# Performance work log

Hardware: AMD Instinct MI355X
Metric: run time of the kernel (lower is better)

The kernel has to match this reference:

```python
import jax, jax.numpy as jnp
import numpy as np

B, N, IN, H, OUT = 128, 8192, 9, 128, 9


def setup_inputs() -> dict:
    key = jax.random.key(0)
    ks = jax.random.split(key, 4)
    y = jax.random.normal(ks[0], (B, N, 6), dtype=jnp.float32)
    W1 = jax.random.normal(ks[1], (IN, H), dtype=jnp.float32) / np.sqrt(IN)
    b1 = jnp.zeros((H,), dtype=jnp.float32)
    W2 = jax.random.normal(ks[2], (H, H), dtype=jnp.float32) / np.sqrt(H)
    b2 = jnp.zeros((H,), dtype=jnp.float32)
    W3 = jax.random.normal(ks[3], (H, OUT), dtype=jnp.float32) / np.sqrt(H)
    b3 = jnp.zeros((OUT,), dtype=jnp.float32)
    return {"y": y, "W1": W1, "b1": b1, "W2": W2, "b2": b2, "W3": W3, "b3": b3}


def _make_triplets(coords):
    # coords: (B, N, 3) -> (B, N-2, 9) = (a1, a2, a3, x1, y1, x2, y2, x3, y3)
    xp = coords[:, :-2, :]
    xm = coords[:, 1:-1, :]
    xn = coords[:, 2:, :]
    off = jnp.arctan2(xm[..., 1] - xp[..., 1], xm[..., 0] - xp[..., 0])
    return jnp.stack(
        (xp[..., 2] - off, xm[..., 2] - off, xn[..., 2] - off,
         xp[..., 0], xp[..., 1], xm[..., 0], xm[..., 1], xn[..., 0], xn[..., 1]),
        axis=-1,
    )


def reference(y, W1, b1, W2, b2, W3, b3):
    coords = y[..., :3]                      # (B, N, 3)
    t = _make_triplets(coords)               # (B, N-2, 9)
    h = jax.nn.swish(t @ W1 + b1)            # (B, N-2, H)
    h = jax.nn.swish(h @ W2 + b2)            # (B, N-2, H)
    f = h @ W3 + b3                          # (B, N-2, 9)
    # overlap-add scatter back onto the N cycles
    res = jnp.zeros_like(coords)
    res = res.at[:, :-2, :].add(jnp.stack([f[..., 3], f[..., 4], f[..., 0]], axis=-1))
    res = res.at[:, 1:-1, :].add(jnp.stack([f[..., 5], f[..., 6], f[..., 1]], axis=-1))
    res = res.at[:, 2:, :].add(jnp.stack([f[..., 7], f[..., 8], f[..., 2]], axis=-1))
    # boundaries = (1, 1): clamp both ends
    res = res.at[:, 0, :].set(0.0)
    res = res.at[:, -1, :].set(0.0)
    return res
```

## Files before the change

kernel.cpp:

```cpp
#include <hip/hip_runtime.h>
#include <hip/hip_bf16.h>

#define Bn 128
#define Nn 8192
#define Hn 128
#define RPB 128
#define JOUT 126
#define NBJ 66

typedef __attribute__((ext_vector_type(8))) short short8;
typedef __attribute__((ext_vector_type(4))) float f32x4;
typedef __attribute__((ext_vector_type(4))) unsigned int u32x4;

__device__ __forceinline__ unsigned short f2bf(float x) {
    union { float f; unsigned u; } v; v.f = x;
    return (unsigned short)((v.u + 0x7fffu + ((v.u >> 16) & 1u)) >> 16);
}
__device__ __forceinline__ float bf2f(unsigned short h) {
    union { unsigned u; float f; } v; v.u = ((unsigned)h) << 16;
    return v.f;
}
__device__ __forceinline__ unsigned short flo(float x) {
    return f2bf(x - bf2f(f2bf(x)));
}
__device__ __forceinline__ float swish(float x) {
    return x * __builtin_amdgcn_rcpf(1.0f + __expf(-x));
}
__device__ __forceinline__ unsigned pk2(float a, float b) {
    union { __hip_bfloat16 h; unsigned short u; } ca, cb;
    ca.h = __float2bfloat16(a); cb.h = __float2bfloat16(b);
    return (unsigned)ca.u | ((unsigned)cb.u << 16);
}

__global__ void prep_kernel(const float* __restrict__ W1, const float* __restrict__ b1,
                            const float* __restrict__ W2, const float* __restrict__ W3,
                            unsigned short* __restrict__ ws)
{
    int tid = blockIdx.x * 256 + threadIdx.x;
    if (tid >= 22528) return;
    int f = tid >> 9, r = tid & 511;
    int l = r >> 3, e = r & 7;
    int p = ((l >> 4) << 3) | e;
    int c16 = l & 15;
    unsigned short v = 0;
    if (f < 8) {
        int col = (f << 4) | c16;
        if (p < 9)        v = f2bf(W1[p * Hn + col]);
        else if (p < 18)  v = flo(W1[(p - 9) * Hn + col]);
        else if (p < 27)  v = f2bf(W1[(p - 18) * Hn + col]);
        else if (p == 27) v = f2bf(b1[col]);
        else if (p == 28) v = flo(b1[col]);
    } else if (f < 40) {
        int mt2 = (f - 8) >> 2, ks = (f - 8) & 3;
        int col = (mt2 << 4) | c16;
        int k = 16 * (2 * ks + ((p & 7) >> 2)) + ((p >> 3) << 2) + (p & 3);
        v = f2bf(W2[k * Hn + col]);
    } else {
        int ks = f - 40;
        int k = 16 * (2 * ks + ((p & 7) >> 2)) + ((p >> 3) << 2) + (p & 3);
        if (c16 < 9) v = f2bf(W3[k * 9 + c16]);
    }
    ws[tid] = v;
}

__global__ __launch_bounds__(256, 4) void fused_kernel(
    const float* __restrict__ y, const float* __restrict__ b2g,
    const float* __restrict__ b3, const unsigned short* __restrict__ ws,
    float* __restrict__ out)
{
    __shared__ __align__(16) char tb[RPB * 80];
    __shared__ float f_lds[RPB][12];

    const int tid = threadIdx.x;
    const int lane = tid & 63;
    const int w = tid >> 6;
    const int b = blockIdx.y;
    const int j0 = blockIdx.x * JOUT;
    const int r15 = lane & 15, g = lane >> 4;

    const short8* wsf = (const short8*)ws;

    if (tid < RPB) {
        int i = j0 - 2 + tid;
        i = (i < 0) ? 0 : ((i > Nn - 3) ? (Nn - 3) : i);
        const float* base = y + ((size_t)b * Nn + i) * 6;
        float xp0 = base[0],  xp1 = base[1],  xp2 = base[2];
        float xm0 = base[6],  xm1 = base[7],  xm2 = base[8];
        float xn0 = base[12], xn1 = base[13], xn2 = base[14];
        float off = atan2f(xm1 - xp1, xm0 - xp0);
        float t0 = xp2 - off, t1 = xm2 - off, t2 = xn2 - off;
        unsigned short h0 = f2bf(t0), h1 = f2bf(t1), h2 = f2bf(t2);
        unsigned short h3 = f2bf(xp0), h4 = f2bf(xp1), h5 = f2bf(xm0);
        unsigned short h6 = f2bf(xm1), h7 = f2bf(xn0), h8 = f2bf(xn1);
        unsigned short l0 = f2bf(t0 - bf2f(h0)), l1 = f2bf(t1 - bf2f(h1));
        unsigned short l2 = f2bf(t2 - bf2f(h2)), l3 = f2bf(xp0 - bf2f(h3));
        unsigned short l4 = f2bf(xp1 - bf2f(h4)), l5 = f2bf(xm0 - bf2f(h5));
        unsigned short l6 = f2bf(xm1 - bf2f(h6)), l7 = f2bf(xn0 - bf2f(h7));
        unsigned short l8 = f2bf(xn1 - bf2f(h8));
        #define PK(a,bv) ((unsigned)(a) | ((unsigned)(bv) << 16))
        u32x4 v0 = { PK(h0,h1), PK(h2,h3), PK(h4,h5), PK(h6,h7) };
        u32x4 v1 = { PK(h8,h0), PK(h1,h2), PK(h3,h4), PK(h5,h6) };
        u32x4 v2 = { PK(h7,h8), PK(l0,l1), PK(l2,l3), PK(l4,l5) };
        u32x4 v3 = { PK(l6,l7), PK(l8,0x3F80u), PK(0x3F80u,0u), 0u };
        #undef PK
        char* dst = tb + tid * 80;
        *(u32x4*)(dst)      = v0;
        *(u32x4*)(dst + 16) = v1;
        *(u32x4*)(dst + 32) = v2;
        *(u32x4*)(dst + 48) = v3;
    }
    __syncthreads();

    short8 b2f[2][4];
    {
        short8 w1f[8];
        #pragma unroll
        for (int mt = 0; mt < 8; ++mt) w1f[mt] = wsf[mt * 64 + lane];
        #pragma unroll
        for (int nt = 0; nt < 2; ++nt) {
            short8 tf = *(const short8*)(tb + (32 * w + 16 * nt + r15) * 80 + g * 16);
            f32x4 acc1[8];
            #pragma unroll
            for (int mt = 0; mt < 8; ++mt)
                acc1[mt] = __builtin_amdgcn_mfma_f32_16x16x32_bf16(w1f[mt], tf, (f32x4)0.0f, 0, 0, 0);
            #pragma unroll
            for (int ks = 0; ks < 4; ++ks) {
                union { unsigned u[4]; short8 s; } pk;
                pk.u[0] = pk2(swish(acc1[2 * ks][0]),     swish(acc1[2 * ks][1]));
                pk.u[1] = pk2(swish(acc1[2 * ks][2]),     swish(acc1[2 * ks][3]));
                pk.u[2] = pk2(swish(acc1[2 * ks + 1][0]), swish(acc1[2 * ks + 1][1]));
                pk.u[3] = pk2(swish(acc1[2 * ks + 1][2]), swish(acc1[2 * ks + 1][3]));
                b2f[nt][ks] = pk.s;
            }
        }
    }

    unsigned a3u[2][4][4];
    #pragma unroll
    for (int mt2 = 0; mt2 < 8; ++mt2) {
        short8 a2f0 = wsf[512 + (mt2 * 4 + 0) * 64 + lane];
        short8 a2f1 = wsf[512 + (mt2 * 4 + 1) * 64 + lane];
        short8 a2f2 = wsf[512 + (mt2 * 4 + 2) * 64 + lane];
        short8 a2f3 = wsf[512 + (mt2 * 4 + 3) * 64 + lane];
        const f32x4 bias = *(const f32x4*)(b2g + mt2 * 16 + 4 * g);
        #pragma unroll
        for (int nt = 0; nt < 2; ++nt) {
            f32x4 acc = __builtin_amdgcn_mfma_f32_16x16x32_bf16(a2f0, b2f[nt][0], (f32x4)0.0f, 0, 0, 0);
            acc = __builtin_amdgcn_mfma_f32_16x16x32_bf16(a2f1, b2f[nt][1], acc, 0, 0, 0);
            acc = __builtin_amdgcn_mfma_f32_16x16x32_bf16(a2f2, b2f[nt][2], acc, 0, 0, 0);
            acc = __builtin_amdgcn_mfma_f32_16x16x32_bf16(a2f3, b2f[nt][3], acc, 0, 0, 0);
            float s0 = swish(acc[0] + bias[0]);
            float s1 = swish(acc[1] + bias[1]);
            float s2 = swish(acc[2] + bias[2]);
            float s3 = swish(acc[3] + bias[3]);
            a3u[nt][mt2 >> 1][(mt2 & 1) * 2 + 0] = pk2(s0, s1);
            a3u[nt][mt2 >> 1][(mt2 & 1) * 2 + 1] = pk2(s2, s3);
        }
    }

    {
        short8 b3f[4];
        #pragma unroll
        for (int ks = 0; ks < 4; ++ks) b3f[ks] = wsf[2560 + ks * 64 + lane];
        float b3v = (r15 < 9) ? b3[r15] : 0.0f;
        #pragma unroll
        for (int nt = 0; nt < 2; ++nt) {
            union { unsigned u[4]; short8 s; } c0, c1, c2, c3;
            #pragma unroll
            for (int q = 0; q < 4; ++q) {
                c0.u[q] = a3u[nt][0][q]; c1.u[q] = a3u[nt][1][q];
                c2.u[q] = a3u[nt][2][q]; c3.u[q] = a3u[nt][3][q];
            }
            f32x4 f01 = __builtin_amdgcn_mfma_f32_16x16x32_bf16(c0.s, b3f[0], (f32x4)0.0f, 0, 0, 0);
            f01 = __builtin_amdgcn_mfma_f32_16x16x32_bf16(c1.s, b3f[1], f01, 0, 0, 0);
            f32x4 f23 = __builtin_amdgcn_mfma_f32_16x16x32_bf16(c2.s, b3f[2], (f32x4)0.0f, 0, 0, 0);
            f23 = __builtin_amdgcn_mfma_f32_16x16x32_bf16(c3.s, b3f[3], f23, 0, 0, 0);
            f32x4 fa = f01 + f23;
            if (r15 < 9) {
                #pragma unroll
                for (int e = 0; e < 4; ++e)
                    f_lds[32 * w + 16 * nt + 4 * g + e][r15] = fa[e] + b3v;
            }
        }
    }
    __syncthreads();

    for (int o = tid; o < 3 * JOUT; o += 256) {
        int jo = o / 3, c = o - jo * 3;
        int j = j0 + jo;
        if (j < Nn) {
            float val = 0.0f;
            if (j != 0 && j != Nn - 1) {
                int cP = (c == 0) ? 3 : (c == 1) ? 4 : 0;
                int cM = (c == 0) ? 5 : (c == 1) ? 6 : 1;
                int cN = (c == 0) ? 7 : (c == 1) ? 8 : 2;
                if (j <= Nn - 3) val += f_lds[jo + 2][cP];
                val += f_lds[jo + 1][cM];
                if (j >= 2) val += f_lds[jo][cN];
            }
            out[((size_t)b * Nn + j) * 3 + c] = val;
        }
    }
}

extern "C" void kernel_launch(void* const* d_in, const int* in_sizes, int n_in,
                              void* d_out, int out_size, void* d_ws, size_t ws_size,
                              hipStream_t stream)
{
    const float* y  = (const float*)d_in[0];
    const float* W1 = (const float*)d_in[1];
    const float* b1 = (const float*)d_in[2];
    const float* W2 = (const float*)d_in[3];
    const float* b2 = (const float*)d_in[4];
    const float* W3 = (const float*)d_in[5];
    const float* b3 = (const float*)d_in[6];
    unsigned short* ws = (unsigned short*)d_ws;
    float* out = (float*)d_out;

    prep_kernel<<<88, 256, 0, stream>>>(W1, b1, W2, W3, ws);
    dim3 grid(NBJ, Bn);
    fused_kernel<<<grid, 256, 0, stream>>>(y, b2, b3, ws, out);
}
```

Before: 106.8 us.

## Process row tiles sequentially and fuse layer-3 MFMA into layer-2 loop

Restructures the per-wave MLP so each of the two 16-row tiles runs through layers 1, 2 and 3 in a non-unrolled loop, rather than carrying both tiles' intermediates across stages. Layer-3 MFMAs are issued right after each pair of layer-2 output tiles, so the full a3u array and the b3f fragments no longer stay live at once. This aims to cut VGPR pressure and raise occupancy, but it gives up interleaving MFMAs from independent tiles and reloads the W1 fragments once per tile.

```diff
diff --git a/kernel.cpp b/kernel.cpp
--- a/kernel.cpp
+++ b/kernel.cpp
@@ -111,13 +111,15 @@
     }
     __syncthreads();
 
-    short8 b2f[2][4];
-    {
-        short8 w1f[8];
-        #pragma unroll
-        for (int mt = 0; mt < 8; ++mt) w1f[mt] = wsf[mt * 64 + lane];
-        #pragma unroll
-        for (int nt = 0; nt < 2; ++nt) {
+    #pragma unroll 1
+    for (int nt = 0; nt < 2; ++nt) {
+        asm volatile("" ::: "memory");
+
+        short8 b2f[4];
+        {
+            short8 w1f[8];
+            #pragma unroll
+            for (int mt = 0; mt < 8; ++mt) w1f[mt] = wsf[mt * 64 + lane];
             short8 tf = *(const short8*)(tb + (32 * w + 16 * nt + r15) * 80 + g * 16);
             f32x4 acc1[8];
             #pragma unroll
@@ -130,57 +132,38 @@
                 pk.u[1] = pk2(swish(acc1[2 * ks][2]),     swish(acc1[2 * ks][3]));
                 pk.u[2] = pk2(swish(acc1[2 * ks + 1][0]), swish(acc1[2 * ks + 1][1]));
                 pk.u[3] = pk2(swish(acc1[2 * ks + 1][2]), swish(acc1[2 * ks + 1][3]));
-                b2f[nt][ks] = pk.s;
+                b2f[ks] = pk.s;
             }
         }
-    }
-
-    unsigned a3u[2][4][4];
-    #pragma unroll
-    for (int mt2 = 0; mt2 < 8; ++mt2) {
-        short8 a2f0 = wsf[512 + (mt2 * 4 + 0) * 64 + lane];
-        short8 a2f1 = wsf[512 + (mt2 * 4 + 1) * 64 + lane];
-        short8 a2f2 = wsf[512 + (mt2 * 4 + 2) * 64 + lane];
-        short8 a2f3 = wsf[512 + (mt2 * 4 + 3) * 64 + lane];
-        const f32x4 bias = *(const f32x4*)(b2g + mt2 * 16 + 4 * g);
+
+        f32x4 facc = (f32x4)0.0f;
         #pragma unroll
-        for (int nt = 0; nt < 2; ++nt) {
-            f32x4 acc = __builtin_amdgcn_mfma_f32_16x16x32_bf16(a2f0, b2f[nt][0], (f32x4)0.0f, 0, 0, 0);
-            acc = __builtin_amdgcn_mfma_f32_16x16x32_bf16(a2f1, b2f[nt][1], acc, 0, 0, 0);
-            acc = __builtin_amdgcn_mfma_f32_16x16x32_bf16(a2f2, b2f[nt][2], acc, 0, 0, 0);
-            acc = __builtin_amdgcn_mfma_f32_16x16x32_bf16(a2f3, b2f[nt][3], acc, 0, 0, 0);
-            float s0 = swish(acc[0] + bias[0]);
-            float s1 = swish(acc[1] + bias[1]);
-            float s2 = swish(acc[2] + bias[2]);
-            float s3 = swish(acc[3] + bias[3]);
-            a3u[nt][mt2 >> 1][(mt2 & 1) * 2 + 0] = pk2(s0, s1);
-            a3u[nt][mt2 >> 1][(mt2 & 1) * 2 + 1] = pk2(s2, s3);
-        }
-    }
-
-    {
-        short8 b3f[4];
-        #pragma unroll
-        for (int ks = 0; ks < 4; ++ks) b3f[ks] = wsf[2560 + ks * 64 + lane];
-        float b3v = (r15 < 9) ? b3[r15] : 0.0f;
-        #pragma unroll
-        for (int nt = 0; nt < 2; ++nt) {
-            union { unsigned u[4]; short8 s; } c0, c1, c2, c3;
-            #pragma unroll
-            for (int q = 0; q < 4; ++q) {
-                c0.u[q] = a3u[nt][0][q]; c1.u[q] = a3u[nt][1][q];
-                c2.u[q] = a3u[nt][2][q]; c3.u[q] = a3u[nt][3][q];
+        for (int i = 0; i < 4; ++i) {
+            union { unsigned u[4]; short8 s; } cc;
+            #pragma unroll
+            for (int h = 0; h < 2; ++h) {
+                const int mt2 = 2 * i + h;
+                short8 a0 = wsf[512 + (mt2 * 4 + 0) * 64 + lane];
+                short8 a1 = wsf[512 + (mt2 * 4 + 1) * 64 + lane];
+                short8 a2 = wsf[512 + (mt2 * 4 + 2) * 64 + lane];
+                short8 a3 = wsf[512 + (mt2 * 4 + 3) * 64 + lane];
+                f32x4 acc = __builtin_amdgcn_mfma_f32_16x16x32_bf16(a0, b2f[0], (f32x4)0.0f, 0, 0, 0);
+                acc = __builtin_amdgcn_mfma_f32_16x16x32_bf16(a1, b2f[1], acc, 0, 0, 0);
+                acc = __builtin_amdgcn_mfma_f32_16x16x32_bf16(a2, b2f[2], acc, 0, 0, 0);
+                acc = __builtin_amdgcn_mfma_f32_16x16x32_bf16(a3, b2f[3], acc, 0, 0, 0);
+                const f32x4 bias = *(const f32x4*)(b2g + mt2 * 16 + 4 * g);
+                cc.u[2 * h + 0] = pk2(swish(acc[0] + bias[0]), swish(acc[1] + bias[1]));
+                cc.u[2 * h + 1] = pk2(swish(acc[2] + bias[2]), swish(acc[3] + bias[3]));
             }
-            f32x4 f01 = __builtin_amdgcn_mfma_f32_16x16x32_bf16(c0.s, b3f[0], (f32x4)0.0f, 0, 0, 0);
-            f01 = __builtin_amdgcn_mfma_f32_16x16x32_bf16(c1.s, b3f[1], f01, 0, 0, 0);
-            f32x4 f23 = __builtin_amdgcn_mfma_f32_16x16x32_bf16(c2.s, b3f[2], (f32x4)0.0f, 0, 0, 0);
-            f23 = __builtin_amdgcn_mfma_f32_16x16x32_bf16(c3.s, b3f[3], f23, 0, 0, 0);
-            f32x4 fa = f01 + f23;
-            if (r15 < 9) {
-                #pragma unroll
-                for (int e = 0; e < 4; ++e)
-                    f_lds[32 * w + 16 * nt + 4 * g + e][r15] = fa[e] + b3v;
-            }
+            short8 b3fi = wsf[2560 + i * 64 + lane];
+            facc = __builtin_amdgcn_mfma_f32_16x16x32_bf16(cc.s, b3fi, facc, 0, 0, 0);
+        }
+
+        if (r15 < 9) {
+            float b3v = b3[r15];
+            #pragma unroll
+            for (int e = 0; e < 4; ++e)
+                f_lds[32 * w + 16 * nt + 4 * g + e][r15] = facc[e] + b3v;
         }
     }
     __syncthreads();
```

Result: slower. 151.5 us (+41.9%).
